# Optimization experiments

Hardware: AMD Instinct MI355X
Metric: run time of the kernel (lower is better)

Reference implementation:

```python
import jax, jax.numpy as jnp
import numpy as np

N, P, K, LF = 1024, 20000, 8, 1  # samples, in_features(=fold_num at stride 1), kernel_size, local_feature


def setup_inputs() -> dict:
    key = jax.random.key(0)
    k1, k2 = jax.random.split(key)
    X = jax.random.normal(k1, (N, P), dtype=jnp.float32)
    # GlorotUniform over weight tensor (fold_num, kernel_size, local_feature)
    limit = np.sqrt(6.0 / (K + LF)).astype(np.float32)
    W = jax.random.uniform(k2, (P, K, LF), dtype=jnp.float32, minval=-limit, maxval=limit)
    b = jnp.zeros((P, LF), dtype=jnp.float32)
    return {"X": X, "W": W, "b": b}


def reference(X, W, b):
    # Pad right by kernel_size-1 (same as tf.pad with [[0,0],[0,K-1]])
    Xp = jnp.pad(X, ((0, 0), (0, K - 1)))  # [N, P+K-1]
    # im2col: sliding windows of length K at stride 1 -> [N, P, K]
    idx = jnp.arange(P)[:, None] + jnp.arange(K)[None, :]  # [P, K]
    patches = Xp[:, idx]  # [N, P, K]
    # per-position matmul with distinct weights W[p] in R^{KxLF}, LF=1
    AL = jnp.einsum('npk,pkl->npl', patches, W) + b  # [N, P, 1]
    return AL.reshape(X.shape[0], P)  # [N, P]
```

## Files before the change

kernel.cpp:

```cpp
#include <hip/hip_runtime.h>


constexpr int N  = 1024;
constexpr int P  = 20000;
constexpr int K  = 8;
constexpr int P4 = P / 4;
constexpr int COLS_PADDED = 5120;
constexpr int NCHUNKS = 128;
constexpr int ROWS = N / NCHUNKS;

typedef float float4n __attribute__((ext_vector_type(4)));

__global__ __launch_bounds__(256)
void transpose_w(const float* __restrict__ W, float* __restrict__ Wt) {
    int p = blockIdx.x * blockDim.x + threadIdx.x;
    if (p >= P) return;
    float4 a = *reinterpret_cast<const float4*>(W + (size_t)p * K);
    float4 c = *reinterpret_cast<const float4*>(W + (size_t)p * K + 4);
    Wt[0 * P + p] = a.x; Wt[1 * P + p] = a.y;
    Wt[2 * P + p] = a.z; Wt[3 * P + p] = a.w;
    Wt[4 * P + p] = c.x; Wt[5 * P + p] = c.y;
    Wt[6 * P + p] = c.z; Wt[7 * P + p] = c.w;
}

__global__ __launch_bounds__(256, 4)
void local_linear_kernel(const float* __restrict__ X,
                         const float* __restrict__ Wt,
                         const float* __restrict__ b,
                         float* __restrict__ out) {
    const int tid   = blockIdx.x * blockDim.x + threadIdx.x;
    const int chunk = tid / COLS_PADDED;
    const int q     = tid - chunk * COLS_PADDED;
    if (q >= P4) return;
    const int p  = q * 4;
    const int n0 = chunk * ROWS;

    float4n wv[8];
    #pragma unroll
    for (int k = 0; k < K; ++k)
        wv[k] = *reinterpret_cast<const float4n*>(Wt + (size_t)k * P + p);
    float4n bv = *reinterpret_cast<const float4n*>(b + p);

    asm volatile("" : "+v"(wv[0]), "+v"(wv[1]), "+v"(wv[2]), "+v"(wv[3]),
                      "+v"(wv[4]), "+v"(wv[5]), "+v"(wv[6]), "+v"(wv[7]),
                      "+v"(bv));

    const bool interior = (p + 12 <= P);

    #pragma unroll 2
    for (int r = 0; r < ROWS; ++r) {
        const float* xrow = X + (size_t)(n0 + r) * P;

        float xv[12];
        if (interior) {
            float4n a = *reinterpret_cast<const float4n*>(xrow + p);
            float4n c = *reinterpret_cast<const float4n*>(xrow + p + 4);
            float4n d = *reinterpret_cast<const float4n*>(xrow + p + 8);
            xv[0] = a.x; xv[1] = a.y; xv[2]  = a.z; xv[3]  = a.w;
            xv[4] = c.x; xv[5] = c.y; xv[6]  = c.z; xv[7]  = c.w;
            xv[8] = d.x; xv[9] = d.y; xv[10] = d.z; xv[11] = d.w;
        } else {
            #pragma unroll
            for (int i = 0; i < 12; ++i)
                xv[i] = (p + i < P) ? xrow[p + i] : 0.0f;
        }

        float r0 = bv.x, r1 = bv.y, r2 = bv.z, r3 = bv.w;
        #pragma unroll
        for (int k = 0; k < K; ++k) {
            r0 += xv[k + 0] * wv[k].x;
            r1 += xv[k + 1] * wv[k].y;
            r2 += xv[k + 2] * wv[k].z;
            r3 += xv[k + 3] * wv[k].w;
        }

        float4n o; o.x = r0; o.y = r1; o.z = r2; o.w = r3;
        __builtin_nontemporal_store(
            o, reinterpret_cast<float4n*>(out + (size_t)(n0 + r) * P + p));
    }
}

extern "C" void kernel_launch(void* const* d_in, const int* in_sizes, int n_in,
                              void* d_out, int out_size, void* d_ws, size_t ws_size,
                              hipStream_t stream) {
    const float* X = (const float*)d_in[0];
    const float* W = (const float*)d_in[1];
    const float* b = (const float*)d_in[2];
    float* out = (float*)d_out;

    constexpr int total_threads = COLS_PADDED * NCHUNKS;
    constexpr int block = 256;
    constexpr int grid = total_threads / block;

    float* Wt = (float*)d_ws;
    transpose_w<<<(P + block - 1) / block, block, 0, stream>>>(W, Wt);
    local_linear_kernel<<<grid, block, 0, stream>>>(X, Wt, b, out);
}
```

Before: 37.36 us.

## Share overlapping X halo across lanes via wavefront shuffles instead of reloads

Each lane now loads only its own float4 of X per row and gets the next two neighbours' values through __shfl_down, instead of issuing three float4 loads per row. Each wave covers 62 column groups with a 2-lane halo, so the grid is re-tiled per wave, and the row loop unroll goes from 2 to 4. This targets redundant global/L2 load traffic for the overlapping windows. The cost is 8 cross-lane shuffles per row and about 3% idle halo lanes. A clamped load address keeps out-of-range lanes safe.

```diff
diff --git a/kernel.cpp b/kernel.cpp
--- a/kernel.cpp
+++ b/kernel.cpp
@@ -5,7 +5,10 @@
 constexpr int P  = 20000;
 constexpr int K  = 8;
 constexpr int P4 = P / 4;
-constexpr int COLS_PADDED = 5120;
+constexpr int GPW = 62;
+constexpr int CWAVES = (P4 + GPW - 1) / GPW;
+constexpr int WPB = 4;
+constexpr int CBLKS = (CWAVES + WPB - 1) / WPB;
 constexpr int NCHUNKS = 128;
 constexpr int ROWS = N / NCHUNKS;
 
@@ -23,42 +26,56 @@
     Wt[6 * P + p] = c.z; Wt[7 * P + p] = c.w;
 }
 
+__device__ __forceinline__ float4n shdn(float4n v, int d) {
+    float4n r;
+    r.x = __shfl_down(v.x, d);
+    r.y = __shfl_down(v.y, d);
+    r.z = __shfl_down(v.z, d);
+    r.w = __shfl_down(v.w, d);
+    return r;
+}
+
 __global__ __launch_bounds__(256, 4)
 void local_linear_kernel(const float* __restrict__ X,
                          const float* __restrict__ Wt,
                          const float* __restrict__ b,
                          float* __restrict__ out) {
-    const int tid   = blockIdx.x * blockDim.x + threadIdx.x;
-    const int chunk = tid / COLS_PADDED;
-    const int q     = tid - chunk * COLS_PADDED;
-    if (q >= P4) return;
-    const int p  = q * 4;
-    const int n0 = chunk * ROWS;
+    const int chunk = blockIdx.x / CBLKS;
+    const int cblk  = blockIdx.x - chunk * CBLKS;
+    const int wid   = threadIdx.x >> 6;
+    const int lane  = threadIdx.x & 63;
+    const int cw    = cblk * WPB + wid;
+    const int q0    = cw * GPW;
+    if (q0 >= P4) return;
+    const int q     = q0 + lane;
+    const int p     = q * 4;
+    const int psafe = (p <= P - 4) ? p : (P - 4);
+    const int n0    = chunk * ROWS;
+    const bool interior = (p + 12 <= P);
+    const bool doStore  = (lane < GPW) && (q < P4);
 
     float4n wv[8];
     #pragma unroll
     for (int k = 0; k < K; ++k)
-        wv[k] = *reinterpret_cast<const float4n*>(Wt + (size_t)k * P + p);
-    float4n bv = *reinterpret_cast<const float4n*>(b + p);
-
+        wv[k] = *reinterpret_cast<const float4n*>(Wt + (size_t)k * P + psafe);
+    float4n bv = *reinterpret_cast<const float4n*>(b + psafe);
     asm volatile("" : "+v"(wv[0]), "+v"(wv[1]), "+v"(wv[2]), "+v"(wv[3]),
                       "+v"(wv[4]), "+v"(wv[5]), "+v"(wv[6]), "+v"(wv[7]),
                       "+v"(bv));
 
-    const bool interior = (p + 12 <= P);
-
-    #pragma unroll 2
+    #pragma unroll 4
     for (int r = 0; r < ROWS; ++r) {
         const float* xrow = X + (size_t)(n0 + r) * P;
 
+        float4n x0 = *reinterpret_cast<const float4n*>(xrow + psafe);
+        float4n x1 = shdn(x0, 1);
+        float4n x2 = shdn(x0, 2);
+
         float xv[12];
         if (interior) {
-            float4n a = *reinterpret_cast<const float4n*>(xrow + p);
-            float4n c = *reinterpret_cast<const float4n*>(xrow + p + 4);
-            float4n d = *reinterpret_cast<const float4n*>(xrow + p + 8);
-            xv[0] = a.x; xv[1] = a.y; xv[2]  = a.z; xv[3]  = a.w;
-            xv[4] = c.x; xv[5] = c.y; xv[6]  = c.z; xv[7]  = c.w;
-            xv[8] = d.x; xv[9] = d.y; xv[10] = d.z; xv[11] = d.w;
+            xv[0] = x0.x; xv[1] = x0.y; xv[2]  = x0.z; xv[3]  = x0.w;
+            xv[4] = x1.x; xv[5] = x1.y; xv[6]  = x1.z; xv[7]  = x1.w;
+            xv[8] = x2.x; xv[9] = x2.y; xv[10] = x2.z; xv[11] = x2.w;
         } else {
             #pragma unroll
             for (int i = 0; i < 12; ++i)
@@ -74,9 +91,11 @@
             r3 += xv[k + 3] * wv[k].w;
         }
 
-        float4n o; o.x = r0; o.y = r1; o.z = r2; o.w = r3;
-        __builtin_nontemporal_store(
-            o, reinterpret_cast<float4n*>(out + (size_t)(n0 + r) * P + p));
+        if (doStore) {
+            float4n o; o.x = r0; o.y = r1; o.z = r2; o.w = r3;
+            __builtin_nontemporal_store(
+                o, reinterpret_cast<float4n*>(out + (size_t)(n0 + r) * P + p));
+        }
     }
 }
 
@@ -88,9 +107,8 @@
     const float* b = (const float*)d_in[2];
     float* out = (float*)d_out;
 
-    constexpr int total_threads = COLS_PADDED * NCHUNKS;
     constexpr int block = 256;
-    constexpr int grid = total_threads / block;
+    constexpr int grid = CBLKS * NCHUNKS;
 
     float* Wt = (float*)d_ws;
     transpose_w<<<(P + block - 1) / block, block, 0, stream>>>(W, Wt);
```

After: 39.32 us. 5.2% more time.
